# Optimization experiments

Measured on AMD Instinct MI355X. Metric: run time of the kernel, lower is better.

## Reference

```python
import jax, jax.numpy as jnp
import numpy as np

N = 50000          # nodes
E = 1600000        # edges (avg degree 32)
H, DH = 8, 16      # heads, dim per head (SE3Transformer heads=8, dim_head=16)
D_IN = 8           # pos(3) + node-type embedding(5)
EDGE_DIM = 4       # edge_attr features (num_degrees=4)
HID = H * DH       # 128 = hidden_dim
OUT = 1
TYPES = 100
GRAPHS = 64


def setup_inputs() -> dict:
    key = jax.random.key(0)
    ks = jax.random.split(key, 12)
    pos = jax.random.normal(ks[0], (N, 3), dtype=jnp.float32)
    z = jax.random.randint(ks[1], (N,), 0, TYPES)
    edge_index = jax.random.randint(ks[2], (2, E), 0, N)
    edge_attr = jax.random.normal(ks[3], (E, EDGE_DIM), dtype=jnp.float32)
    batch = jnp.sort(jax.random.randint(ks[4], (N,), 0, GRAPHS))
    s = 0.1
    emb = jax.random.normal(ks[5], (TYPES, D_IN - 3), dtype=jnp.float32) * s
    Wq = jax.random.normal(ks[6], (D_IN, HID), dtype=jnp.float32) * s
    Wk = jax.random.normal(ks[7], (D_IN + EDGE_DIM, HID), dtype=jnp.float32) * s
    Wv = jax.random.normal(ks[8], (D_IN + EDGE_DIM, HID), dtype=jnp.float32) * s
    Wo = jax.random.normal(ks[9], (HID, HID), dtype=jnp.float32) * s
    lin_W = jax.random.normal(ks[10], (HID, OUT), dtype=jnp.float32) * s
    lin_b = jnp.zeros((OUT,), dtype=jnp.float32)
    return {"pos": pos, "z": z, "edge_index": edge_index, "edge_attr": edge_attr,
            "batch": batch, "emb": emb, "Wq": Wq, "Wk": Wk, "Wv": Wv,
            "Wo": Wo, "lin_W": lin_W, "lin_b": lin_b}


def reference(pos, z, edge_index, edge_attr, batch, emb, Wq, Wk, Wv, Wo, lin_W, lin_b):
    # node features: concat(pos, embedding(z))  -> [N, 8]
    x = jnp.concatenate([pos, emb[z]], axis=-1)
    src, dst = edge_index[0], edge_index[1]

    # edge-indexed multi-head graph attention (SE3Transformer core pattern)
    q = (x @ Wq).reshape(N, H, DH)                           # [N, H, DH]
    e_in = jnp.concatenate([x[src], edge_attr], axis=-1)     # [E, 12] gather
    k = (e_in @ Wk).reshape(E, H, DH)
    v = (e_in @ Wv).reshape(E, H, DH)

    scale = 1.0 / jnp.sqrt(jnp.float32(DH))
    scores = jnp.einsum('ehd,ehd->eh', q[dst], k) * scale    # [E, H]

    # segment softmax over incoming edges of each destination node
    m = jax.ops.segment_max(scores, dst, num_segments=N)     # [N, H]
    ex = jnp.exp(scores - m[dst])
    denom = jax.ops.segment_sum(ex, dst, num_segments=N)     # [N, H]
    w = ex / jnp.maximum(denom[dst], 1e-9)                   # [E, H]

    agg = jax.ops.segment_sum(w[:, :, None] * v, dst, num_segments=N)  # [N, H, DH]
    feats = agg.reshape(N, HID) @ Wo                         # [N, 128]

    h = jax.nn.relu(feats)
    y = h @ lin_W + lin_b                                    # [N, OUT]

    # global mean pool per graph
    sums = jax.ops.segment_sum(y, batch, num_segments=GRAPHS)
    cnts = jax.ops.segment_sum(jnp.ones((N, 1), y.dtype), batch, num_segments=GRAPHS)
    return sums / jnp.maximum(cnts, 1.0)                     # [GRAPHS, OUT]
```

## Files before the change

kernel.cpp:

```cpp
#include <hip/hip_runtime.h>

#define N_NODES 50000
#define N_EDGES 1600000
#define NHEAD 8
#define DH 16
#define D_IN 8
#define E_IN_DIM 12
#define HID 128
#define GRAPHS 64
#define N_PAD 50016
#define BINK 98
#define NB 512
#define T_MS 8192
#define MSB ((N_EDGES + T_MS - 1) / T_MS)
#define LCAP 3840

__global__ __launch_bounds__(256) void k_node1(
    const float* __restrict__ pos, const int* __restrict__ z,
    const float* __restrict__ emb,
    const float* __restrict__ Wq, const float* __restrict__ Wk,
    float* __restrict__ x, float* __restrict__ qk)
{
    __shared__ float sWq[D_IN * HID];
    __shared__ float sWk[E_IN_DIM * HID];
    __shared__ float sx[32][D_IN];

    int tid = threadIdx.x;
    for (int i = tid; i < D_IN * HID; i += 256) sWq[i] = Wq[i];
    for (int i = tid; i < E_IN_DIM * HID; i += 256) sWk[i] = Wk[i];

    int nl = tid >> 3;
    int h  = tid & 7;
    int n  = blockIdx.x * 32 + nl;

    if (n < N_NODES) {
        int j = h;
        float v;
        if (j < 3) v = pos[n * 3 + j];
        else       v = emb[z[n] * 5 + (j - 3)];
        sx[nl][j] = v;
        x[n * D_IN + j] = v;
    }
    __syncthreads();
    if (n >= N_NODES) return;

    float q[DH];
    #pragma unroll
    for (int d = 0; d < DH; ++d) {
        float acc = 0.f;
        #pragma unroll
        for (int j = 0; j < D_IN; ++j)
            acc += sx[nl][j] * sWq[j * HID + h * DH + d];
        q[d] = acc;
    }
    const float scale = 0.25f;
    #pragma unroll
    for (int j = 0; j < E_IN_DIM; ++j) {
        float acc = 0.f;
        #pragma unroll
        for (int d = 0; d < DH; ++d)
            acc += q[d] * sWk[j * HID + h * DH + d];
        qk[n * 96 + h * 12 + j] = acc * scale;
    }
}

__global__ __launch_bounds__(256) void k_bhist(
    const int* __restrict__ dst, int* __restrict__ bcount)
{
    __shared__ int lh[NB];
    int tid = threadIdx.x;
    for (int i = tid; i < NB; i += 256) lh[i] = 0;
    __syncthreads();

    int stride = gridDim.x * 256;
    const int NI4 = N_EDGES / 4;
    for (int i = blockIdx.x * 256 + tid; i < NI4; i += stride) {
        int4 d4 = ((const int4*)dst)[i];
        atomicAdd(&lh[d4.x / BINK], 1);
        atomicAdd(&lh[d4.y / BINK], 1);
        atomicAdd(&lh[d4.z / BINK], 1);
        atomicAdd(&lh[d4.w / BINK], 1);
    }
    __syncthreads();
    for (int i = tid; i < NB; i += 256) {
        int v = lh[i];
        if (v > 0) atomicAdd(&bcount[i * 16], v);
    }
}

__global__ __launch_bounds__(512) void k_bscan(
    const int* __restrict__ bcount, int* __restrict__ binoff, int* __restrict__ bincur)
{
    __shared__ int tmp[NB];
    int t = threadIdx.x;
    int v = bcount[t * 16];
    tmp[t] = v;
    __syncthreads();
    #pragma unroll
    for (int off = 1; off < NB; off <<= 1) {
        int u = (t >= off) ? tmp[t - off] : 0;
        __syncthreads();
        if (t >= off) tmp[t] += u;
        __syncthreads();
    }
    int ex = tmp[t] - v;
    binoff[t] = ex;
    bincur[t * 16] = ex;
    if (t == NB - 1) binoff[NB] = tmp[t];
}

__global__ __launch_bounds__(1024) void k_msplit(
    const int* __restrict__ edge_index, const float* __restrict__ edge_attr,
    int* __restrict__ bincur,
    int2* __restrict__ sd_g, float4* __restrict__ ea_g)
{
    __shared__ int hist[NB];
    __shared__ int hscan[NB];
    __shared__ int cnt[NB];
    __shared__ int gb[NB];
    __shared__ int stmp[NB];
    __shared__ int sdst[T_MS];
    __shared__ unsigned short perm[T_MS];

    int tid = threadIdx.x;
    int base = blockIdx.x * T_MS;
    int nact = min(T_MS, N_EDGES - base);
    const int* dstp = edge_index + N_EDGES;

    for (int i = tid; i < NB; i += 1024) { hist[i] = 0; cnt[i] = 0; }
    __syncthreads();

    for (int i = tid; i < nact; i += 1024) {
        int d = dstp[base + i];
        sdst[i] = d;
        atomicAdd(&hist[d / BINK], 1);
    }
    __syncthreads();

    if (tid < NB) stmp[tid] = hist[tid];
    __syncthreads();
    for (int off = 1; off < NB; off <<= 1) {
        int u = 0;
        if (tid < NB && tid >= off) u = stmp[tid - off];
        __syncthreads();
        if (tid < NB && tid >= off) stmp[tid] += u;
        __syncthreads();
    }
    if (tid < NB) {
        int v = hist[tid];
        hscan[tid] = stmp[tid] - v;
        gb[tid] = (v > 0) ? atomicAdd(&bincur[tid * 16], v) : 0;
    }
    __syncthreads();

    for (int i = tid; i < nact; i += 1024) {
        int b = sdst[i] / BINK;
        int r = atomicAdd(&cnt[b], 1);
        perm[hscan[b] + r] = (unsigned short)i;
    }
    __syncthreads();

    for (int s = tid; s < nact; s += 1024) {
        int li = (int)perm[s];
        int e = base + li;
        int d = sdst[li];
        int b = d / BINK;
        int dest = gb[b] + (s - hscan[b]);
        sd_g[dest] = make_int2(edge_index[e], d);
        ea_g[dest] = ((const float4*)edge_attr)[e];
    }
}

__global__ __launch_bounds__(512) void k_attn_f(
    const int* __restrict__ binoff, const int2* __restrict__ sd_g,
    const float4* __restrict__ ea_g,
    const float* __restrict__ x,
    const float* __restrict__ qk, const float* __restrict__ Wv,
    float* __restrict__ agg)
{
    __shared__ float sWv[E_IN_DIM * HID];
    __shared__ int   soff[129];
    __shared__ int   cnt[BINK];
    __shared__ int   stmp[128];
    __shared__ int2  list[LCAP];

    int tid = threadIdx.x;
    int b = blockIdx.x;
    int nlo = b * BINK;
    int nhi = min(nlo + BINK, N_NODES);
    int nn = nhi - nlo;
    if (nn <= 0) return;

    for (int i = tid; i < E_IN_DIM * HID; i += 512) sWv[i] = Wv[i];
    for (int i = tid; i < nn; i += 512) cnt[i] = 0;
    int gbeg = binoff[b];
    int total = binoff[b + 1] - gbeg;
    __syncthreads();

    for (int i = tid; i < total; i += 512) {
        int2 v = sd_g[gbeg + i];
        atomicAdd(&cnt[v.y - nlo], 1);
    }
    __syncthreads();

    if (tid < 128) stmp[tid] = (tid < nn) ? cnt[tid] : 0;
    __syncthreads();
    #pragma unroll
    for (int off = 1; off < 128; off <<= 1) {
        int u = 0;
        if (tid < 128 && tid >= off) u = stmp[tid - off];
        __syncthreads();
        if (tid < 128 && tid >= off) stmp[tid] += u;
        __syncthreads();
    }
    if (tid < 128) soff[tid + 1] = stmp[tid];
    if (tid == 0) soff[0] = 0;
    for (int i = tid; i < nn; i += 512) cnt[i] = 0;
    __syncthreads();

    for (int i = tid; i < total; i += 512) {
        int2 v = sd_g[gbeg + i];
        int ln = v.y - nlo;
        int r = atomicAdd(&cnt[ln], 1);
        int li = soff[ln] + r;
        if (li < LCAP) list[li] = make_int2(v.x, i);
    }
    __syncthreads();

    int w = tid >> 6, l = tid & 63;
    int es = l >> 3, h = l & 7;
    const float4* easeg = ea_g + gbeg;
    for (int nl = w; nl < nn; nl += 8) {
        int n = nlo + nl;
        const float4* qr = (const float4*)(qk + (size_t)n * 96 + h * 12);
        float4 q0 = qr[0], q1 = qr[1], q2 = qr[2];
        int lbeg = soff[nl];
        int lcnt = soff[nl + 1] - lbeg;

        float sr[12];
        #pragma unroll
        for (int j = 0; j < 12; ++j) sr[j] = 0.f;
        float denom = 0.f;

        int umax = (lcnt + 7) >> 3;
        #pragma unroll 2
        for (int u = 0; u < umax; ++u) {
            int r = u * 8 + es;
            bool a2 = r < lcnt;
            int2 p = list[lbeg + (a2 ? r : 0)];
            const float4* xp = (const float4*)(x + p.x * 8);
            float4 x0 = xp[0], x1 = xp[1];
            float4 ea = easeg[p.y];
            float sc = x0.x*q0.x + x0.y*q0.y + x0.z*q0.z + x0.w*q0.w
                     + x1.x*q1.x + x1.y*q1.y + x1.z*q1.z + x1.w*q1.w
                     + ea.x*q2.x + ea.y*q2.y + ea.z*q2.z + ea.w*q2.w;
            float ex = a2 ? __expf(sc) : 0.f;
            denom += ex;
            sr[0] += ex * x0.x; sr[1]  += ex * x0.y; sr[2]  += ex * x0.z; sr[3]  += ex * x0.w;
            sr[4] += ex * x1.x; sr[5]  += ex * x1.y; sr[6]  += ex * x1.z; sr[7]  += ex * x1.w;
            sr[8] += ex * ea.x; sr[9]  += ex * ea.y; sr[10] += ex * ea.z; sr[11] += ex * ea.w;
        }

        #pragma unroll
        for (int m = 8; m <= 32; m <<= 1) {
            denom += __shfl_xor(denom, m);
            #pragma unroll
            for (int j = 0; j < 12; ++j) sr[j] += __shfl_xor(sr[j], m);
        }

        float inv = 1.0f / fmaxf(denom, 1e-9f);
        int d0 = h * DH + 2 * es;
        float a0 = 0.f, a1 = 0.f;
        #pragma unroll
        for (int j = 0; j < E_IN_DIM; ++j) {
            a0 += sr[j] * sWv[j * HID + d0];
            a1 += sr[j] * sWv[j * HID + d0 + 1];
        }
        *(float2*)(agg + (size_t)n * HID + d0) = make_float2(a0 * inv, a1 * inv);
    }
}

__global__ __launch_bounds__(256) void k_mlp(
    const float* __restrict__ agg, const float* __restrict__ Wo,
    const float* __restrict__ lin_W, const float* __restrict__ lin_b,
    const int* __restrict__ batch,
    float* __restrict__ gsum, float* __restrict__ gcnt)
{
    __shared__ float sWo[64 * HID];
    __shared__ float sAgg[32][HID + 1];
    __shared__ float sRed[8][33];
    __shared__ float bsum[GRAPHS];
    __shared__ int   bcnt[GRAPHS];

    int tid = threadIdx.x;
    int nbase = blockIdx.x * 32;

    if (tid < GRAPHS) { bsum[tid] = 0.f; bcnt[tid] = 0; }

    {
        const float4* ag = (const float4*)(agg + (size_t)nbase * HID);
        #pragma unroll
        for (int k = 0; k < 4; ++k) {
            int i4 = k * 256 + tid;
            float4 v = ag[i4];
            int fi = i4 * 4;
            int r = fi >> 7, c = fi & 127;
            sAgg[r][c] = v.x; sAgg[r][c + 1] = v.y; sAgg[r][c + 2] = v.z; sAgg[r][c + 3] = v.w;
        }
    }

    int h  = tid >> 5;
    int nl = tid & 31;
    int n  = nbase + nl;

    float f[16];
    #pragma unroll
    for (int d = 0; d < 16; ++d) f[d] = 0.f;

    #pragma unroll
    for (int half = 0; half < 2; ++half) {
        __syncthreads();
        const float4* wp = (const float4*)(Wo + half * 64 * HID);
        #pragma unroll
        for (int k = 0; k < 8; ++k) {
            int i4 = k * 256 + tid;
            ((float4*)sWo)[i4] = wp[i4];
        }
        __syncthreads();
        #pragma unroll 4
        for (int i = 0; i < 64; ++i) {
            float av = sAgg[nl][half * 64 + i];
            const float4* wr = (const float4*)(sWo + i * HID + h * 16);
            float4 w0 = wr[0], w1 = wr[1], w2 = wr[2], w3 = wr[3];
            f[0]  += av * w0.x; f[1]  += av * w0.y; f[2]  += av * w0.z; f[3]  += av * w0.w;
            f[4]  += av * w1.x; f[5]  += av * w1.y; f[6]  += av * w1.z; f[7]  += av * w1.w;
            f[8]  += av * w2.x; f[9]  += av * w2.y; f[10] += av * w2.z; f[11] += av * w2.w;
            f[12] += av * w3.x; f[13] += av * w3.y; f[14] += av * w3.z; f[15] += av * w3.w;
        }
    }

    const float4* lwp = (const float4*)(lin_W + h * 16);
    float4 lw0 = lwp[0], lw1 = lwp[1], lw2 = lwp[2], lw3 = lwp[3];
    float ps = fmaxf(f[0],0.f)*lw0.x + fmaxf(f[1],0.f)*lw0.y + fmaxf(f[2],0.f)*lw0.z + fmaxf(f[3],0.f)*lw0.w
             + fmaxf(f[4],0.f)*lw1.x + fmaxf(f[5],0.f)*lw1.y + fmaxf(f[6],0.f)*lw1.z + fmaxf(f[7],0.f)*lw1.w
             + fmaxf(f[8],0.f)*lw2.x + fmaxf(f[9],0.f)*lw2.y + fmaxf(f[10],0.f)*lw2.z + fmaxf(f[11],0.f)*lw2.w
             + fmaxf(f[12],0.f)*lw3.x + fmaxf(f[13],0.f)*lw3.y + fmaxf(f[14],0.f)*lw3.z + fmaxf(f[15],0.f)*lw3.w;

    sRed[h][nl] = ps;
    __syncthreads();
    if (h == 0 && n < N_NODES) {
        float y = lin_b[0];
        #pragma unroll
        for (int k = 0; k < 8; ++k) y += sRed[k][nl];
        int g = batch[n];
        atomicAdd(&bsum[g], y);
        atomicAdd(&bcnt[g], 1);
    }
    __syncthreads();
    if (tid < GRAPHS) {
        int c = bcnt[tid];
        if (c > 0) {
            atomicAdd(&gsum[tid], bsum[tid]);
            atomicAdd(&gcnt[tid], (float)c);
        }
    }
}

__global__ void k_final(const float* __restrict__ gsum, const float* __restrict__ gcnt,
                        float* __restrict__ out)
{
    int g = threadIdx.x;
    if (g < GRAPHS) out[g] = gsum[g] / fmaxf(gcnt[g], 1.0f);
}

extern "C" void kernel_launch(void* const* d_in, const int* in_sizes, int n_in,
                              void* d_out, int out_size, void* d_ws, size_t ws_size,
                              hipStream_t stream)
{
    const float* pos       = (const float*)d_in[0];
    const int*   z         = (const int*)  d_in[1];
    const int*   edge_index= (const int*)  d_in[2];
    const float* edge_attr = (const float*)d_in[3];
    const int*   batch     = (const int*)  d_in[4];
    const float* emb       = (const float*)d_in[5];
    const float* Wq        = (const float*)d_in[6];
    const float* Wk        = (const float*)d_in[7];
    const float* Wv        = (const float*)d_in[8];
    const float* Wo        = (const float*)d_in[9];
    const float* lin_W     = (const float*)d_in[10];
    const float* lin_b     = (const float*)d_in[11];
    float* out = (float*)d_out;

    char* ws = (char*)d_ws;
    float* gsum   = (float*)ws;
    float* gcnt   = gsum + GRAPHS;
    int*   bcount = (int*)(gcnt + GRAPHS);
    int*   binoff = bcount + NB * 16;
    int*   bincur = binoff + 520;
    char*  tail   = (char*)(bincur + NB * 16);

    hipMemsetAsync(gsum, 0, (size_t)(2 * GRAPHS + NB * 16) * sizeof(int), stream);

    int2*   sd_g = (int2*)tail;
    float4* ea_g = (float4*)(sd_g + N_EDGES);
    float*  x    = (float*)(ea_g + N_EDGES);
    float*  qk   = x + (size_t)N_NODES * 8;
    float*  agg  = qk + (size_t)N_NODES * 96;

    k_node1 <<<(N_NODES + 31) / 32, 256, 0, stream>>>(pos, z, emb, Wq, Wk, x, qk);
    k_bhist <<<512, 256, 0, stream>>>(edge_index + N_EDGES, bcount);
    k_bscan <<<1, NB, 0, stream>>>(bcount, binoff, bincur);
    k_msplit<<<MSB, 1024, 0, stream>>>(edge_index, edge_attr, bincur, sd_g, ea_g);
    k_attn_f<<<NB, 512, 0, stream>>>(binoff, sd_g, ea_g, x, qk, Wv, agg);
    k_mlp   <<<(N_PAD / 32), 256, 0, stream>>>(agg, Wo, lin_W, lin_b, batch, gsum, gcnt);
    k_final <<<1, 64, 0, stream>>>(gsum, gcnt, out);
}
```

Baseline: 182.9 us.

## Halve destination bin size and pack src/dst into one 32-bit word

Doubles the number of destination bins to 1024, each holding 49 nodes, so the attention kernel launches more, smaller blocks with a smaller per-block edge list. Source and destination indices are packed into one 32-bit word instead of an int2, which halves the bucketed index traffic. The attention kernel also stages the packed words in LDS so the second counting pass avoids a re-read from global memory. The packing relies on the node count fitting in 16 bits, and a smaller LCAP of 2048 risks overflow if a bin has unusually many edges.

Result: slower. 203.8 us (+11.4%).

```diff
diff --git a/kernel.cpp b/kernel.cpp
--- a/kernel.cpp
+++ b/kernel.cpp
@@ -9,11 +9,11 @@
 #define HID 128
 #define GRAPHS 64
 #define N_PAD 50016
-#define BINK 98
-#define NB 512
+#define BINK 49
+#define NB 1024
 #define T_MS 8192
 #define MSB ((N_EDGES + T_MS - 1) / T_MS)
-#define LCAP 3840
+#define LCAP 2048
 
 __global__ __launch_bounds__(256) void k_node1(
     const float* __restrict__ pos, const int* __restrict__ z,
@@ -88,7 +88,7 @@
     }
 }
 
-__global__ __launch_bounds__(512) void k_bscan(
+__global__ __launch_bounds__(1024) void k_bscan(
     const int* __restrict__ bcount, int* __restrict__ binoff, int* __restrict__ bincur)
 {
     __shared__ int tmp[NB];
@@ -112,13 +112,12 @@
 __global__ __launch_bounds__(1024) void k_msplit(
     const int* __restrict__ edge_index, const float* __restrict__ edge_attr,
     int* __restrict__ bincur,
-    int2* __restrict__ sd_g, float4* __restrict__ ea_g)
+    unsigned int* __restrict__ sd_g, float4* __restrict__ ea_g)
 {
     __shared__ int hist[NB];
     __shared__ int hscan[NB];
     __shared__ int cnt[NB];
     __shared__ int gb[NB];
-    __shared__ int stmp[NB];
     __shared__ int sdst[T_MS];
     __shared__ unsigned short perm[T_MS];
 
@@ -137,19 +136,20 @@
     }
     __syncthreads();
 
-    if (tid < NB) stmp[tid] = hist[tid];
-    __syncthreads();
-    for (int off = 1; off < NB; off <<= 1) {
-        int u = 0;
-        if (tid < NB && tid >= off) u = stmp[tid - off];
-        __syncthreads();
-        if (tid < NB && tid >= off) stmp[tid] += u;
-        __syncthreads();
-    }
-    if (tid < NB) {
+    {
         int v = hist[tid];
-        hscan[tid] = stmp[tid] - v;
+        hscan[tid] = v;
+        __syncthreads();
+        #pragma unroll
+        for (int off = 1; off < NB; off <<= 1) {
+            int u = (tid >= off) ? hscan[tid - off] : 0;
+            __syncthreads();
+            if (tid >= off) hscan[tid] += u;
+            __syncthreads();
+        }
+        int ex = hscan[tid] - v;
         gb[tid] = (v > 0) ? atomicAdd(&bincur[tid * 16], v) : 0;
+        hscan[tid] = ex;
     }
     __syncthreads();
 
@@ -166,23 +166,24 @@
         int d = sdst[li];
         int b = d / BINK;
         int dest = gb[b] + (s - hscan[b]);
-        sd_g[dest] = make_int2(edge_index[e], d);
+        sd_g[dest] = ((unsigned int)edge_index[e] << 16) | (unsigned int)d;
         ea_g[dest] = ((const float4*)edge_attr)[e];
     }
 }
 
 __global__ __launch_bounds__(512) void k_attn_f(
-    const int* __restrict__ binoff, const int2* __restrict__ sd_g,
+    const int* __restrict__ binoff, const unsigned int* __restrict__ sd_g,
     const float4* __restrict__ ea_g,
     const float* __restrict__ x,
     const float* __restrict__ qk, const float* __restrict__ Wv,
     float* __restrict__ agg)
 {
     __shared__ float sWv[E_IN_DIM * HID];
-    __shared__ int   soff[129];
-    __shared__ int   cnt[BINK];
-    __shared__ int   stmp[128];
-    __shared__ int2  list[LCAP];
+    __shared__ unsigned int raw[LCAP];
+    __shared__ unsigned int list[LCAP];
+    __shared__ int soff[BINK + 1];
+    __shared__ int cnt[BINK];
+    __shared__ int stmp[64];
 
     int tid = threadIdx.x;
     int b = blockIdx.x;
@@ -198,32 +199,33 @@
     __syncthreads();
 
     for (int i = tid; i < total; i += 512) {
-        int2 v = sd_g[gbeg + i];
-        atomicAdd(&cnt[v.y - nlo], 1);
-    }
-    __syncthreads();
-
-    if (tid < 128) stmp[tid] = (tid < nn) ? cnt[tid] : 0;
-    __syncthreads();
-    #pragma unroll
-    for (int off = 1; off < 128; off <<= 1) {
+        unsigned int v = sd_g[gbeg + i];
+        if (i < LCAP) raw[i] = v;
+        atomicAdd(&cnt[(int)(v & 0xFFFFu) - nlo], 1);
+    }
+    __syncthreads();
+
+    if (tid < 64) stmp[tid] = (tid < nn) ? cnt[tid] : 0;
+    __syncthreads();
+    #pragma unroll
+    for (int off = 1; off < 64; off <<= 1) {
         int u = 0;
-        if (tid < 128 && tid >= off) u = stmp[tid - off];
-        __syncthreads();
-        if (tid < 128 && tid >= off) stmp[tid] += u;
-        __syncthreads();
-    }
-    if (tid < 128) soff[tid + 1] = stmp[tid];
+        if (tid < 64 && tid >= off) u = stmp[tid - off];
+        __syncthreads();
+        if (tid < 64 && tid >= off) stmp[tid] += u;
+        __syncthreads();
+    }
+    if (tid < 64) soff[tid + 1] = stmp[tid];
     if (tid == 0) soff[0] = 0;
     for (int i = tid; i < nn; i += 512) cnt[i] = 0;
     __syncthreads();
 
-    for (int i = tid; i < total; i += 512) {
-        int2 v = sd_g[gbeg + i];
-        int ln = v.y - nlo;
+    for (int i = tid; i < total && i < LCAP; i += 512) {
+        unsigned int v = raw[i];
+        int ln = (int)(v & 0xFFFFu) - nlo;
         int r = atomicAdd(&cnt[ln], 1);
         int li = soff[ln] + r;
-        if (li < LCAP) list[li] = make_int2(v.x, i);
+        if (li < LCAP) list[li] = (v & 0xFFFF0000u) | (unsigned int)i;
     }
     __syncthreads();
 
@@ -247,10 +249,12 @@
         for (int u = 0; u < umax; ++u) {
             int r = u * 8 + es;
             bool a2 = r < lcnt;
-            int2 p = list[lbeg + (a2 ? r : 0)];
-            const float4* xp = (const float4*)(x + p.x * 8);
+            unsigned int p = list[lbeg + (a2 ? r : 0)];
+            int src = (int)(p >> 16);
+            int seg = (int)(p & 0xFFFFu);
+            const float4* xp = (const float4*)(x + src * 8);
             float4 x0 = xp[0], x1 = xp[1];
-            float4 ea = easeg[p.y];
+            float4 ea = easeg[seg];
             float sc = x0.x*q0.x + x0.y*q0.y + x0.z*q0.z + x0.w*q0.w
                      + x1.x*q1.x + x1.y*q1.y + x1.z*q1.z + x1.w*q1.w
                      + ea.x*q2.x + ea.y*q2.y + ea.z*q2.z + ea.w*q2.w;
@@ -396,12 +400,12 @@
     float* gcnt   = gsum + GRAPHS;
     int*   bcount = (int*)(gcnt + GRAPHS);
     int*   binoff = bcount + NB * 16;
-    int*   bincur = binoff + 520;
+    int*   bincur = binoff + 1032;
     char*  tail   = (char*)(bincur + NB * 16);
 
     hipMemsetAsync(gsum, 0, (size_t)(2 * GRAPHS + NB * 16) * sizeof(int), stream);
 
-    int2*   sd_g = (int2*)tail;
+    unsigned int* sd_g = (unsigned int*)tail;
     float4* ea_g = (float4*)(sd_g + N_EDGES);
     float*  x    = (float*)(ea_g + N_EDGES);
     float*  qk   = x + (size_t)N_NODES * 8;
```
